# Kernel tuning notes

Measured on AMD Instinct MI355X. Metric: run time of the kernel, lower is better.

The kernel has to match this reference:

```python
import math
import jax, jax.numpy as jnp
import numpy as np
from jax import lax

FEATURE_DIM = 1024
EMBED_DIM = 300
VOCAB = 32000
HIDDEN = 512
BATCH = 64
MAX_LEN = 40
S = 3  # number of feature maps summed in l_total


def setup_inputs() -> dict:
    key = jax.random.key(0)
    ks = jax.random.split(key, 10)
    l_total = jax.random.normal(ks[0], (S, BATCH, FEATURE_DIM), jnp.float32)
    encoded_captions = jax.random.randint(ks[1], (BATCH, MAX_LEN), 0, VOCAB)
    lengths = jax.random.randint(ks[2], (BATCH,), 5, MAX_LEN + 1)
    lengths = lengths.at[0].set(MAX_LEN)  # ensure max(decode_lengths) == MAX_LEN-1 (static)
    caption_lengths = lengths[:, None]
    # parameters (per PlainDecoder.init_weights / torch defaults)
    emb_weight = jax.random.uniform(ks[3], (VOCAB, EMBED_DIM), jnp.float32, -0.1, 0.1)
    k = 1.0 / math.sqrt(HIDDEN)
    W_ih = jax.random.uniform(ks[4], (4 * HIDDEN, EMBED_DIM + FEATURE_DIM), jnp.float32, -k, k)
    W_hh = jax.random.uniform(ks[5], (4 * HIDDEN, HIDDEN), jnp.float32, -k, k)
    b_ih = jax.random.uniform(ks[6], (4 * HIDDEN,), jnp.float32, -k, k)
    b_hh = jax.random.uniform(ks[7], (4 * HIDDEN,), jnp.float32, -k, k)
    wdc_W = jax.random.uniform(ks[8], (VOCAB, HIDDEN), jnp.float32, -0.1, 0.1)
    wdc_b = jnp.zeros((VOCAB,), jnp.float32)
    return {
        "l_total": l_total,
        "encoded_captions": encoded_captions,
        "caption_lengths": caption_lengths,
        "emb_weight": emb_weight,
        "W_ih": W_ih,
        "W_hh": W_hh,
        "b_ih": b_ih,
        "b_hh": b_hh,
        "wdc_W": wdc_W,
        "wdc_b": wdc_b,
    }


def reference(l_total, encoded_captions, caption_lengths, emb_weight, W_ih, W_hh, b_ih, b_hh, wdc_W, wdc_b):
    # l_total: (S, B, F) -> permute(1,2,0).sum(-1) -> (B, F)
    lt = jnp.transpose(l_total, (1, 2, 0)).sum(-1)
    lengths = caption_lengths[:, 0]
    sort_ind = jnp.argsort(-lengths)  # descending
    lengths_s = lengths[sort_ind]
    lt = lt[sort_ind]
    caps = encoded_captions[sort_ind]
    decode_lengths = lengths_s - 1
    embeds = emb_weight[caps]  # (B, L, E)

    T = caps.shape[1] - 1  # static max decode length (max length pinned in setup)
    B = caps.shape[0]
    H = W_hh.shape[1]

    emb_seq = jnp.transpose(embeds[:, :T, :], (1, 0, 2))  # (T, B, E)
    mask = jnp.arange(T)[:, None] < decode_lengths[None, :]  # (T, B)

    def step(carry, xs):
        h, c = carry
        emb_t, mask_t = xs
        x = jnp.concatenate([emb_t, lt], axis=1)  # (B, E+F)
        gates = x @ W_ih.T + h @ W_hh.T + b_ih + b_hh  # (B, 4H)
        i, f, g, o = jnp.split(gates, 4, axis=1)  # torch gate order: i,f,g,o
        i = jax.nn.sigmoid(i)
        f = jax.nn.sigmoid(f)
        g = jnp.tanh(g)
        o = jax.nn.sigmoid(o)
        c = f * c + i * g
        h = o * jnp.tanh(c)
        pred = h @ wdc_W.T + wdc_b  # (B, V)
        pred = jnp.where(mask_t[:, None], pred, jnp.zeros((), pred.dtype))
        return (h, c), pred

    h0 = jnp.zeros((B, H), lt.dtype)
    c0 = jnp.zeros((B, H), lt.dtype)
    _, preds = lax.scan(step, (h0, c0), (emb_seq, mask))  # (T, B, V)
    predictions = jnp.transpose(preds, (1, 0, 2))  # (B, T, V)
    return predictions, caps, decode_lengths, sort_ind
```

## Files before the change

### kernel.cpp

```cpp
#include <hip/hip_runtime.h>
#include <hip/hip_bf16.h>
#include <math.h>

typedef float f32x4 __attribute__((ext_vector_type(4)));
typedef __bf16 bf16x8 __attribute__((ext_vector_type(8)));
typedef __bf16 bf16x4 __attribute__((ext_vector_type(4)));
typedef unsigned long long u64;

#define BATCH   64
#define TSTEPS  39
#define HID     512
#define GATES   2048
#define NVOCAB  32000
#define EMBD    300
#define FEAT    1024
#define XDIM    1324

#define PRED_ELEMS (BATCH*TSTEPS*NVOCAB)

#define NT_M 20
#define NT_N 250
#define TOT_TILES (NT_M*NT_N)
#define REC_BLOCKS 64
#define GRID_BLOCKS 256

#define WS_STEPDONE 0
#define WS_TILECNT  128
#define WS_SORT     256
#define WS_DECLEN   512
#define WS_CAPS     1024
#define WS_BAR      16384
#define WS_LT       65536
#define WS_CONST    327680
#define WS_XP       1048576
#define WS_HALL     22020096
#define WS_WDCB     25165824

__device__ __forceinline__ u64 agent_load_u64(const u64* p) {
    return __hip_atomic_load(p, __ATOMIC_RELAXED, __HIP_MEMORY_SCOPE_AGENT);
}
__device__ __forceinline__ unsigned int agent_load_u32(const unsigned int* p) {
    return __hip_atomic_load(p, __ATOMIC_RELAXED, __HIP_MEMORY_SCOPE_AGENT);
}
__device__ __forceinline__ void agent_store_u32(unsigned int* p, unsigned int v) {
    __hip_atomic_store(p, v, __ATOMIC_RELAXED, __HIP_MEMORY_SCOPE_AGENT);
}

__global__ void k0_setup(const int* caplen, const int* enc,
                         float* out_caps, float* out_declen, float* out_sort,
                         int* ws_sort, int* ws_declen, int* ws_caps,
                         unsigned int* step_done, unsigned int* tile_cnt,
                         unsigned int* bar) {
    __shared__ int L[BATCH];
    __shared__ int sind[BATCH];
    int tid = threadIdx.x;
    if (tid == 0) { *step_done = 0u; *tile_cnt = 0u; }
    for (int x = tid; x < 64*32; x += blockDim.x) bar[x] = 0u;
    if (tid < BATCH) L[tid] = caplen[tid];
    __syncthreads();
    if (tid < BATCH) {
        int len = L[tid];
        int rank = 0;
        for (int j = 0; j < BATCH; ++j) {
            int lj = L[j];
            if (lj > len || (lj == len && j < tid)) rank++;
        }
        sind[rank] = tid;
    }
    __syncthreads();
    if (tid < BATCH) {
        int src = sind[tid];
        ws_sort[tid] = src;
        int dl = L[src] - 1;
        ws_declen[tid] = dl;
        out_declen[tid] = (float)dl;
        out_sort[tid] = (float)src;
    }
    __syncthreads();
    for (int x = tid; x < BATCH*40; x += blockDim.x) {
        int b = x / 40, t = x % 40;
        int v = enc[sind[b]*40 + t];
        ws_caps[x] = v;
        out_caps[x] = (float)v;
    }
}

__global__ void k1_lt(const float* l_total, const int* ws_sort, float* lt) {
    int b = blockIdx.x;
    int ob = ws_sort[b];
    for (int k4 = threadIdx.x; k4 < FEAT/4; k4 += blockDim.x) {
        float4 a = ((const float4*)(l_total + (0*BATCH + ob)*FEAT))[k4];
        float4 c = ((const float4*)(l_total + (1*BATCH + ob)*FEAT))[k4];
        float4 d = ((const float4*)(l_total + (2*BATCH + ob)*FEAT))[k4];
        float4 r;
        r.x = a.x + c.x + d.x;  r.y = a.y + c.y + d.y;
        r.z = a.z + c.z + d.z;  r.w = a.w + c.w + d.w;
        ((float4*)(lt + b*FEAT))[k4] = r;
    }
}

__global__ void k2_const(const float* W_ih, const float* lt,
                         const float* b_ih, const float* b_hh, float* cst) {
    __shared__ float As[32][68];
    __shared__ float Bs[32][36];
    int ctile = blockIdx.x;
    int btile = blockIdx.y;
    int tid = threadIdx.x;
    int ty = tid >> 4, tx = tid & 15;
    float acc[4][2] = {};
    for (int kc = 0; kc < 32; ++kc) {
        __syncthreads();
        #pragma unroll
        for (int j = 0; j < 8; ++j) {
            int idx = tid + j*256;
            int c = idx >> 5, k = idx & 31;
            As[k][c] = W_ih[(ctile*64 + c)*XDIM + 300 + kc*32 + k];
        }
        #pragma unroll
        for (int j = 0; j < 4; ++j) {
            int idx = tid + j*256;
            int b = idx >> 5, k = idx & 31;
            Bs[k][b] = lt[(btile*32 + b)*FEAT + kc*32 + k];
        }
        __syncthreads();
        for (int k = 0; k < 32; ++k) {
            float4 av = *(const float4*)&As[k][ty*4];
            float2 bv = *(const float2*)&Bs[k][tx*2];
            acc[0][0] += av.x*bv.x; acc[0][1] += av.x*bv.y;
            acc[1][0] += av.y*bv.x; acc[1][1] += av.y*bv.y;
            acc[2][0] += av.z*bv.x; acc[2][1] += av.z*bv.y;
            acc[3][0] += av.w*bv.x; acc[3][1] += av.w*bv.y;
        }
    }
    #pragma unroll
    for (int i = 0; i < 4; ++i) {
        int cg = ctile*64 + ty*4 + i;
        float bias = b_ih[cg] + b_hh[cg];
        float2 o;
        o.x = acc[i][0] + bias; o.y = acc[i][1] + bias;
        *(float2*)&cst[cg*64 + btile*32 + tx*2] = o;
    }
}

__global__ void k3_xp(const float* W_ih, const float* emb, const int* ws_caps,
                      const float* cst, float* Xp) {
    __shared__ float As[20][68];
    __shared__ float Bs[20][68];
    int ctile = blockIdx.x;
    int t = blockIdx.y;
    int tid = threadIdx.x;
    int ty = tid >> 4, tx = tid & 15;
    float acc[4][4] = {};
    for (int kc = 0; kc < 15; ++kc) {
        __syncthreads();
        #pragma unroll
        for (int j = 0; j < 5; ++j) {
            int idx = tid + j*256;
            int c = idx / 20, k = idx % 20;
            As[k][c] = W_ih[(ctile*64 + c)*XDIM + kc*20 + k];
        }
        #pragma unroll
        for (int j = 0; j < 5; ++j) {
            int idx = tid + j*256;
            int b = idx / 20, k = idx % 20;
            int tok = ws_caps[b*40 + t];
            Bs[k][b] = emb[tok*EMBD + kc*20 + k];
        }
        __syncthreads();
        for (int k = 0; k < 20; ++k) {
            float4 av = *(const float4*)&As[k][ty*4];
            float4 bv = *(const float4*)&Bs[k][tx*4];
            acc[0][0] += av.x*bv.x; acc[0][1] += av.x*bv.y; acc[0][2] += av.x*bv.z; acc[0][3] += av.x*bv.w;
            acc[1][0] += av.y*bv.x; acc[1][1] += av.y*bv.y; acc[1][2] += av.y*bv.z; acc[1][3] += av.y*bv.w;
            acc[2][0] += av.z*bv.x; acc[2][1] += av.z*bv.y; acc[2][2] += av.z*bv.z; acc[2][3] += av.z*bv.w;
            acc[3][0] += av.w*bv.x; acc[3][1] += av.w*bv.y; acc[3][2] += av.w*bv.z; acc[3][3] += av.w*bv.w;
        }
    }
    #pragma unroll
    for (int i = 0; i < 4; ++i) {
        int cg = ctile*64 + ty*4 + i;
        float4 cs = *(const float4*)&cst[cg*64 + tx*4];
        float4 o;
        o.x = acc[i][0] + cs.x; o.y = acc[i][1] + cs.y;
        o.z = acc[i][2] + cs.z; o.w = acc[i][3] + cs.w;
        *(float4*)&Xp[(t*GATES + cg)*64 + tx*4] = o;
    }
}

__global__ void k4_cvt(const float* wdc, __bf16* wdcb) {
    int n4 = NVOCAB*HID/4;
    for (int i = blockIdx.x*blockDim.x + threadIdx.x; i < n4; i += gridDim.x*blockDim.x) {
        float4 v = ((const float4*)wdc)[i];
        bf16x4 o;
        o[0] = (__bf16)v.x; o[1] = (__bf16)v.y; o[2] = (__bf16)v.z; o[3] = (__bf16)v.w;
        ((bf16x4*)wdcb)[i] = o;
    }
}

__global__ void __launch_bounds__(256) k5_fused(const float* W_hh, const float* Xp,
                                                __bf16* h_all, unsigned int* bar,
                                                unsigned int* step_done, unsigned int* tile_cnt,
                                                const __bf16* wdcb, const float* wdc_b,
                                                const int* ws_declen, float* out) {
    __shared__ __align__(16) char lds_raw[20480];
    __shared__ unsigned int tile_sh;
    int tid = threadIdx.x;
    int l = tid & 63, w = tid >> 6;

    if (blockIdx.x < REC_BLOCKS) {
        float (*gates_lds)[64] = (float(*)[64])(lds_raw);
        float (*c_lds)[64]     = (float(*)[64])(lds_raw + 8192);
        __bf16 (*h_s)[8]       = (__bf16(*)[8])(lds_raw + 10240);
        int p = blockIdx.x;

        __builtin_amdgcn_s_setprio(1);

        bf16x8 wfrag[2][16];
        #pragma unroll
        for (int mt = 0; mt < 2; ++mt) {
            int rr = mt*16 + (l & 15);
            int grow = (rr >> 3)*HID + p*8 + (rr & 7);
            const float* wrow = W_hh + grow*HID;
            #pragma unroll
            for (int kc = 0; kc < 16; ++kc) {
                int k0 = kc*32 + (l >> 4)*8;
                float4 f0 = *(const float4*)(wrow + k0);
                float4 f1 = *(const float4*)(wrow + k0 + 4);
                bf16x8 v;
                v[0]=(__bf16)f0.x; v[1]=(__bf16)f0.y; v[2]=(__bf16)f0.z; v[3]=(__bf16)f0.w;
                v[4]=(__bf16)f1.x; v[5]=(__bf16)f1.y; v[6]=(__bf16)f1.z; v[7]=(__bf16)f1.w;
                wfrag[mt][kc] = v;
            }
        }
        for (int x = tid; x < 8*64; x += 256) ((float*)c_lds)[x] = 0.0f;
        __syncthreads();

        int ulA = tid >> 6;
        int bA  = tid & 63;

        for (int t = 0; t < TSTEPS; ++t) {
            float xg[2][4];
            {
                const float* xpt = Xp + (size_t)t*GATES*64;
                int u0 = p*8 + ulA;
                #pragma unroll
                for (int g = 0; g < 4; ++g) {
                    xg[0][g] = xpt[((size_t)g*512 + u0    )*64 + bA];
                    xg[1][g] = xpt[((size_t)g*512 + u0 + 4)*64 + bA];
                }
            }

            if (t == 0) {
                for (int x = tid; x < 32*64; x += 256) ((float*)gates_lds)[x] = 0.0f;
            } else {
                int bb = w*16 + (l & 15);
                const u64* hq = (const u64*)(h_all + (size_t)(t-1)*BATCH*HID + bb*HID + (l >> 4)*8);
                u64 hl[16][2];
                #pragma unroll
                for (int kc = 0; kc < 16; ++kc) {
                    hl[kc][0] = agent_load_u64(hq + kc*8);
                    hl[kc][1] = agent_load_u64(hq + kc*8 + 1);
                }
                f32x4 acc0 = {0.f,0.f,0.f,0.f};
                f32x4 acc1 = {0.f,0.f,0.f,0.f};
                #pragma unroll
                for (int kc = 0; kc < 16; ++kc) {
                    union { bf16x8 v; u64 u[2]; } uu;
                    uu.u[0] = hl[kc][0]; uu.u[1] = hl[kc][1];
                    acc0 = __builtin_amdgcn_mfma_f32_16x16x32_bf16(wfrag[0][kc], uu.v, acc0, 0, 0, 0);
                    acc1 = __builtin_amdgcn_mfma_f32_16x16x32_bf16(wfrag[1][kc], uu.v, acc1, 0, 0, 0);
                }
                #pragma unroll
                for (int j = 0; j < 4; ++j) {
                    gates_lds[(l>>4)*4 + j][bb]      = acc0[j];
                    gates_lds[16 + (l>>4)*4 + j][bb] = acc1[j];
                }
            }
            __syncthreads();

            #pragma unroll
            for (int half = 0; half < 2; ++half) {
                int ul = ulA + half*4;
                int b  = bA;
                float gi = gates_lds[ul][b]      + xg[half][0];
                float gf = gates_lds[8+ul][b]    + xg[half][1];
                float gg = gates_lds[16+ul][b]   + xg[half][2];
                float go = gates_lds[24+ul][b]   + xg[half][3];
                float ig = 1.0f/(1.0f + expf(-gi));
                float fg = 1.0f/(1.0f + expf(-gf));
                float gv = tanhf(gg);
                float og = 1.0f/(1.0f + expf(-go));
                float c = fg * c_lds[ul][b] + ig * gv;
                c_lds[ul][b] = c;
                float h = og * tanhf(c);
                h_s[b][ul] = (__bf16)h;
            }
            __syncthreads();

            {
                int row = tid >> 2, seg = tid & 3;
                unsigned int val = ((const unsigned int*)&h_s[0][0])[row*4 + seg];
                unsigned int* dst = (unsigned int*)(h_all + ((size_t)t*BATCH + row)*HID + p*8);
                agent_store_u32(dst + seg, val);
            }
            __syncthreads();

            unsigned int tgt = (unsigned int)(t + 1);
            if (tid == 0) agent_store_u32(bar + p*32, tgt);
            if (t < TSTEPS - 1 || p == 0) {
                if (tid < 64) {
                    while (agent_load_u32(bar + tid*32) < tgt)
                        __builtin_amdgcn_s_sleep(1);
                    asm volatile("" ::: "memory");
                    if (p == 0 && tid == 0) agent_store_u32(step_done, tgt);
                }
                __syncthreads();
            }
        }
        __builtin_amdgcn_s_setprio(0);
    }

    {
        __bf16 (*As)[40] = (__bf16(*)[40])(lds_raw);
        __bf16 (*Bs)[40] = (__bf16(*)[40])(lds_raw + 10240);
        int wm = (w >> 1), wn = (w & 1);

        for (;;) {
            if (tid == 0)
                tile_sh = __hip_atomic_fetch_add(tile_cnt, 1u, __ATOMIC_RELAXED,
                                                 __HIP_MEMORY_SCOPE_AGENT);
            __syncthreads();
            unsigned int tile = tile_sh;
            __syncthreads();
            if (tile >= TOT_TILES) break;
            int mtile = tile / NT_N;
            int ntile = tile % NT_N;
            int thi = (mtile*128 + 127) >> 6;
            if (thi > TSTEPS - 1) thi = TSTEPS - 1;
            unsigned int need = (unsigned int)(thi + 1);
            if (tid == 0) {
                while (agent_load_u32(step_done) < need)
                    __builtin_amdgcn_s_sleep(8);
            }
            __syncthreads();
            asm volatile("" ::: "memory");

            f32x4 acc[4][4];
            #pragma unroll
            for (int i = 0; i < 4; ++i)
                #pragma unroll
                for (int j = 0; j < 4; ++j)
                    acc[i][j] = (f32x4){0.f,0.f,0.f,0.f};

            for (int kc = 0; kc < 16; ++kc) {
                __syncthreads();
                #pragma unroll
                for (int j = 0; j < 2; ++j) {
                    int idx = tid + j*256;
                    int row = idx >> 2, seg = idx & 3;
                    int rg = mtile*128 + row;
                    bf16x8 v;
                    if (rg < TSTEPS*BATCH) {
                        v = *(const bf16x8*)(h_all + (size_t)rg*HID + kc*32 + seg*8);
                    } else {
                        #pragma unroll
                        for (int q = 0; q < 8; ++q) v[q] = (__bf16)0.0f;
                    }
                    *(bf16x8*)&As[row][seg*8] = v;
                    int cg = ntile*128 + row;
                    *(bf16x8*)&Bs[row][seg*8] = *(const bf16x8*)(wdcb + (size_t)cg*HID + kc*32 + seg*8);
                }
                __syncthreads();
                bf16x8 af[4], bf[4];
                #pragma unroll
                for (int s = 0; s < 4; ++s) {
                    af[s] = *(const bf16x8*)&As[wm*64 + s*16 + (l & 15)][(l >> 4)*8];
                    bf[s] = *(const bf16x8*)&Bs[wn*64 + s*16 + (l & 15)][(l >> 4)*8];
                }
                #pragma unroll
                for (int sm = 0; sm < 4; ++sm)
                    #pragma unroll
                    for (int sn = 0; sn < 4; ++sn)
                        acc[sm][sn] = __builtin_amdgcn_mfma_f32_16x16x32_bf16(af[sm], bf[sn], acc[sm][sn], 0, 0, 0);
            }

            #pragma unroll
            for (int sm = 0; sm < 4; ++sm) {
                #pragma unroll
                for (int j = 0; j < 4; ++j) {
                    int R = mtile*128 + wm*64 + sm*16 + (l >> 4)*4 + j;
                    if (R >= TSTEPS*BATCH) continue;
                    int t = R >> 6, b = R & 63;
                    int dl = ws_declen[b];
                    #pragma unroll
                    for (int sn = 0; sn < 4; ++sn) {
                        int C = ntile*128 + wn*64 + sn*16 + (l & 15);
                        float v = (t < dl) ? (acc[sm][sn][j] + wdc_b[C]) : 0.0f;
                        out[((size_t)b*TSTEPS + t)*NVOCAB + C] = v;
                    }
                }
            }
            __syncthreads();
        }
    }
}

extern "C" void kernel_launch(void* const* d_in, const int* in_sizes, int n_in,
                              void* d_out, int out_size, void* d_ws, size_t ws_size,
                              hipStream_t stream) {
    const float* l_total = (const float*)d_in[0];
    const int*   enc     = (const int*)d_in[1];
    const int*   caplen  = (const int*)d_in[2];
    const float* emb     = (const float*)d_in[3];
    const float* W_ih    = (const float*)d_in[4];
    const float* W_hh    = (const float*)d_in[5];
    const float* b_ih    = (const float*)d_in[6];
    const float* b_hh    = (const float*)d_in[7];
    const float* wdc_W   = (const float*)d_in[8];
    const float* wdc_b   = (const float*)d_in[9];

    float* out = (float*)d_out;
    char* ws = (char*)d_ws;

    unsigned int* step_done = (unsigned int*)(ws + WS_STEPDONE);
    unsigned int* tile_cnt  = (unsigned int*)(ws + WS_TILECNT);
    unsigned int* bar       = (unsigned int*)(ws + WS_BAR);
    int* ws_sort        = (int*)(ws + WS_SORT);
    int* ws_declen      = (int*)(ws + WS_DECLEN);
    int* ws_caps        = (int*)(ws + WS_CAPS);
    float* lt           = (float*)(ws + WS_LT);
    float* cst          = (float*)(ws + WS_CONST);
    float* Xp           = (float*)(ws + WS_XP);
    __bf16* h_all       = (__bf16*)(ws + WS_HALL);
    __bf16* wdcb        = (__bf16*)(ws + WS_WDCB);

    float* out_caps   = out + PRED_ELEMS;
    float* out_declen = out_caps + BATCH*40;
    float* out_sort   = out_declen + BATCH;

    k0_setup<<<1, 256, 0, stream>>>(caplen, enc, out_caps, out_declen, out_sort,
                                    ws_sort, ws_declen, ws_caps,
                                    step_done, tile_cnt, bar);
    k1_lt<<<BATCH, 256, 0, stream>>>(l_total, ws_sort, lt);
    k2_const<<<dim3(32, 2), 256, 0, stream>>>(W_ih, lt, b_ih, b_hh, cst);
    k3_xp<<<dim3(32, TSTEPS), 256, 0, stream>>>(W_ih, emb, ws_caps, cst, Xp);
    k4_cvt<<<2048, 256, 0, stream>>>(wdc_W, wdcb);
    k5_fused<<<GRID_BLOCKS, 256, 0, stream>>>(W_hh, Xp, h_all, bar,
                                              step_done, tile_cnt,
                                              wdcb, wdc_b, ws_declen, out);
}
```

Measured before the change: 940.0 us.

## Prefetch next K-chunk into registers and double grid block count

```diff
diff --git a/kernel.cpp b/kernel.cpp
--- a/kernel.cpp
+++ b/kernel.cpp
@@ -17,12 +17,13 @@
 #define XDIM    1324
 
 #define PRED_ELEMS (BATCH*TSTEPS*NVOCAB)
+#define MROWS (TSTEPS*BATCH)
 
 #define NT_M 20
 #define NT_N 250
 #define TOT_TILES (NT_M*NT_N)
 #define REC_BLOCKS 64
-#define GRID_BLOCKS 256
+#define GRID_BLOCKS 512
 
 #define WS_STEPDONE 0
 #define WS_TILECNT  128
@@ -345,6 +346,24 @@
             __syncthreads();
             asm volatile("" ::: "memory");
 
+            int seg = tid & 3, row0 = tid >> 2;
+            int rg0 = mtile*128 + row0;
+            const __bf16* hb0 = h_all + (size_t)rg0*HID + seg*8;
+            const __bf16* wb0 = wdcb + (size_t)(ntile*128 + row0)*HID + seg*8;
+
+            bf16x8 zerov;
+            #pragma unroll
+            for (int q = 0; q < 8; ++q) zerov[q] = (__bf16)0.0f;
+
+            bf16x8 a0, a1, b0, b1;
+            auto LK = [&](int kc) {
+                a0 = (rg0      < MROWS) ? *(const bf16x8*)(hb0 + kc*32)                  : zerov;
+                a1 = (rg0 + 64 < MROWS) ? *(const bf16x8*)(hb0 + (size_t)64*HID + kc*32) : zerov;
+                b0 = *(const bf16x8*)(wb0 + kc*32);
+                b1 = *(const bf16x8*)(wb0 + (size_t)64*HID + kc*32);
+            };
+            LK(0);
+
             f32x4 acc[4][4];
             #pragma unroll
             for (int i = 0; i < 4; ++i)
@@ -354,23 +373,12 @@
 
             for (int kc = 0; kc < 16; ++kc) {
                 __syncthreads();
-                #pragma unroll
-                for (int j = 0; j < 2; ++j) {
-                    int idx = tid + j*256;
-                    int row = idx >> 2, seg = idx & 3;
-                    int rg = mtile*128 + row;
-                    bf16x8 v;
-                    if (rg < TSTEPS*BATCH) {
-                        v = *(const bf16x8*)(h_all + (size_t)rg*HID + kc*32 + seg*8);
-                    } else {
-                        #pragma unroll
-                        for (int q = 0; q < 8; ++q) v[q] = (__bf16)0.0f;
-                    }
-                    *(bf16x8*)&As[row][seg*8] = v;
-                    int cg = ntile*128 + row;
-                    *(bf16x8*)&Bs[row][seg*8] = *(const bf16x8*)(wdcb + (size_t)cg*HID + kc*32 + seg*8);
-                }
+                *(bf16x8*)&As[row0][seg*8]      = a0;
+                *(bf16x8*)&As[row0 + 64][seg*8] = a1;
+                *(bf16x8*)&Bs[row0][seg*8]      = b0;
+                *(bf16x8*)&Bs[row0 + 64][seg*8] = b1;
                 __syncthreads();
+                if (kc < 15) LK(kc + 1);
                 bf16x8 af[4], bf[4];
                 #pragma unroll
                 for (int s = 0; s < 4; ++s) {
@@ -389,7 +397,7 @@
                 #pragma unroll
                 for (int j = 0; j < 4; ++j) {
                     int R = mtile*128 + wm*64 + sm*16 + (l >> 4)*4 + j;
-                    if (R >= TSTEPS*BATCH) continue;
+                    if (R >= MROWS) continue;
                     int t = R >> 6, b = R & 63;
                     int dl = ws_declen[b];
                     #pragma unroll
```

Result: faster. 874.1 us (-7.0%).
